# Optimization experiments

Hardware: AMD Instinct MI355X
Metric: run time of the kernel (lower is better)

## Reference

```python
import jax, jax.numpy as jnp
import numpy as np

N_NODES = 1024  # must equal 2*out_channels due to readout(x.T)
N_EDGES = 524288
IN_C, HID_C, OUT_C = 64, 128, 512
MLP_H = 64  # hidden width of EdgeConv MLP


def _linear_init(key, fan_in, fan_out):
    # xavier-normal-like init
    std = (2.0 / (fan_in + fan_out)) ** 0.5
    return jax.random.normal(key, (fan_in, fan_out), dtype=jnp.float32) * std


def setup_inputs() -> dict:
    key = jax.random.key(0)
    ks = jax.random.split(key, 8)
    x = jax.random.normal(ks[0], (N_NODES, IN_C), dtype=jnp.float32)
    edge_index = jax.random.randint(ks[1], (2, N_EDGES), 0, N_NODES, dtype=jnp.int64)
    # conv1 MLP: Linear(2*IN_C, 64) -> ReLU -> Linear(64, HID_C)
    W1 = _linear_init(ks[2], 2 * IN_C, MLP_H); b1 = jnp.zeros((MLP_H,), jnp.float32)
    W2 = _linear_init(ks[3], MLP_H, HID_C);    b2 = jnp.zeros((HID_C,), jnp.float32)
    # conv2 MLP: Linear(2*HID_C, 64) -> ReLU -> Linear(64, OUT_C)
    W3 = _linear_init(ks[4], 2 * HID_C, MLP_H); b3 = jnp.zeros((MLP_H,), jnp.float32)
    W4 = _linear_init(ks[5], MLP_H, OUT_C);     b4 = jnp.zeros((OUT_C,), jnp.float32)
    # readout: Linear(2*OUT_C, OUT_C) applied to x.T (requires N_NODES == 2*OUT_C)
    Wr = _linear_init(ks[6], 2 * OUT_C, OUT_C); br = jnp.zeros((OUT_C,), jnp.float32)
    return {"x": x, "edge_index": edge_index,
            "W1": W1, "b1": b1, "W2": W2, "b2": b2,
            "W3": W3, "b3": b3, "W4": W4, "b4": b4,
            "Wr": Wr, "br": br}


def _edge_conv(x, src, dst, Wa, ba, Wb, bb):
    # message: mlp(cat[x_i, x_j])  with i=target (dst), j=source (src)
    e = jnp.concatenate([x[dst], x[src]], axis=-1)          # [E, 2C]
    m = jnp.maximum(e @ Wa + ba, 0.0) @ Wb + bb             # [E, C_out]
    agg = jax.ops.segment_max(m, dst, num_segments=N_NODES)  # max-aggregate per target node
    # nodes with no incoming edges -> 0 (PyG fill behavior)
    return jnp.where(jnp.isneginf(agg), 0.0, agg)


def reference(x, edge_index, W1, b1, W2, b2, W3, b3, W4, b4, Wr, br):
    src = edge_index[0]
    dst = edge_index[1]
    h = _edge_conv(x, src, dst, W1, b1, W2, b2)   # [N, HID_C]
    h = _edge_conv(h, src, dst, W3, b3, W4, b4)   # [N, OUT_C]
    # readout on h.T: [OUT_C, N] @ [N(=2*OUT_C), OUT_C] -> [OUT_C, OUT_C]
    return h.T @ Wr + br
```

## Files before the change

### kernel.cpp

```cpp
#include <hip/hip_runtime.h>
#include <hip/hip_bf16.h>
#include <float.h>
#include <math.h>

#define N_NODES 1024
#define N_EDGES 524288
#define IN_C    64
#define HID_C   128
#define OUT_C   512
#define MLP_H   64
#define ADJ_WORDS 32
#define KSPLIT  4
#define KCHUNK  (N_NODES / KSPLIT)

typedef __attribute__((ext_vector_type(8))) short short8;
typedef __attribute__((ext_vector_type(4))) float f32x4;

static __device__ __forceinline__ unsigned short f2bf(float f) {
    __hip_bfloat16 h = __float2bfloat16(f);
    return __builtin_bit_cast(unsigned short, h);
}

__global__ void k_zero_adj(unsigned int* __restrict__ adj) {
    int i = blockIdx.x * blockDim.x + threadIdx.x;
    if (i < N_NODES * ADJ_WORDS) adj[i] = 0u;
}

__global__ void k_build_adj(const int* __restrict__ ei, unsigned int* __restrict__ adj) {
    int e = blockIdx.x * blockDim.x + threadIdx.x;
    if (e >= N_EDGES) return;
    int src = ei[e];
    int dst = ei[N_EDGES + e];
    atomicOr(&adj[dst * ADJ_WORDS + (src >> 5)], 1u << (src & 31));
}

__global__ void k_pack_w(const float* __restrict__ W, unsigned short* __restrict__ Wpk, int C) {
    int idx = blockIdx.x * blockDim.x + threadIdx.x;
    int total = (C / 16) * 2 * 64;
    if (idx >= total) return;
    int lane = idx & 63;
    int kf = (idx >> 6) & 1;
    int nt = idx >> 7;
    int kbase = kf * 32 + (lane >> 4) * 8;
    int c = nt * 16 + (lane & 15);
#pragma unroll
    for (int e = 0; e < 8; ++e)
        Wpk[idx * 8 + e] = f2bf(W[(kbase + e) * C + c]);
}

__global__ void k_xform1(const float* __restrict__ x, const float* __restrict__ W1,
                         const float* __restrict__ b1,
                         float* __restrict__ A1, float* __restrict__ B1) {
    int n = blockIdx.x, t = threadIdx.x;
    __shared__ float xs[IN_C];
    xs[t] = x[n * IN_C + t];
    __syncthreads();
    float a = b1[t], b = 0.f;
#pragma unroll
    for (int k = 0; k < IN_C; ++k) {
        float xv = xs[k];
        a = fmaf(xv, W1[k * MLP_H + t], a);
        b = fmaf(xv, W1[(IN_C + k) * MLP_H + t], b);
    }
    A1[n * MLP_H + t] = a;
    B1[n * MLP_H + t] = b;
}

__global__ void k_xform2(const float* __restrict__ h1, const float* __restrict__ W3,
                         const float* __restrict__ b3,
                         float* __restrict__ A2, float* __restrict__ B2) {
    int n = blockIdx.x, t = threadIdx.x;
    __shared__ float hs[HID_C];
    hs[t] = h1[n * HID_C + t];
    hs[t + 64] = h1[n * HID_C + t + 64];
    __syncthreads();
    float a = b3[t], b = 0.f;
#pragma unroll
    for (int k = 0; k < HID_C; ++k) {
        float hv = hs[k];
        a = fmaf(hv, W3[k * MLP_H + t], a);
        b = fmaf(hv, W3[(HID_C + k) * MLP_H + t], b);
    }
    A2[n * MLP_H + t] = a;
    B2[n * MLP_H + t] = b;
}

template <int NTILES, int C_TOTAL>
__global__ __launch_bounds__(256, (NTILES == 2 ? 5 : 4)) void k_conv_mfma(
        const unsigned int* __restrict__ adj,
        const float* __restrict__ Anode, const float* __restrict__ Bnode,
        const unsigned short* __restrict__ Wpk, const float* __restrict__ bias_g,
        float* __restrict__ out) {
    constexpr int BATCH = 4;
    __shared__ unsigned short list[N_NODES + 16];
    __shared__ short8 zbuf[2][BATCH][2][64];
    __shared__ int cnt;
    const int i = blockIdx.x;
    const int tid = threadIdx.x;
    const int lane = tid & 63;
    const int wave = tid >> 6;
    const int g = lane >> 4;
    const int r = lane & 15;

    if (wave == 0) {
        unsigned int bits = (lane < ADJ_WORDS) ? adj[i * ADJ_WORDS + lane] : 0u;
        int c = __popc(bits);
        int pre = c;
#pragma unroll
        for (int d = 1; d < 64; d <<= 1) {
            int t = __shfl_up(pre, d);
            if (lane >= d) pre += t;
        }
        int total = __shfl(pre, 63);
        int pos = pre - c + lane * 0;
        while (bits) {
            int b = __ffs(bits) - 1;
            bits &= bits - 1;
            list[pos++] = (unsigned short)(lane * 32 + b);
        }
        if (lane == 0) cnt = total;
    }
    __syncthreads();
    const int deg = cnt;

    if (deg == 0) {
        if (lane < 16) {
#pragma unroll
            for (int n = 0; n < NTILES; ++n)
                out[i * C_TOTAL + (wave * NTILES + n) * 16 + lane] = 0.f;
        }
        return;
    }

    const int padded = (deg + 15) & ~15;
    for (int p = deg + tid; p < padded; p += 256) list[p] = list[0];

    short8 wfr[NTILES][2];
#pragma unroll
    for (int n = 0; n < NTILES; ++n) {
        int nt = wave * NTILES + n;
#pragma unroll
        for (int kf = 0; kf < 2; ++kf)
            wfr[n][kf] = ((const short8*)Wpk)[(nt * 2 + kf) * 64 + lane];
    }

    const f32x4* Ap = (const f32x4*)(Anode + i * MLP_H);
    f32x4 a0 = Ap[g * 2], a1 = Ap[g * 2 + 1], a2 = Ap[8 + g * 2], a3 = Ap[9 + g * 2];

    float mx[NTILES];
#pragma unroll
    for (int n = 0; n < NTILES; ++n) mx[n] = -INFINITY;

    auto build = [&](int buf, int base_tile, int ntl) {
        if (wave < ntl) {
            int j = list[(base_tile + wave) * 16 + r];
            const f32x4* Bp = (const f32x4*)(Bnode + (size_t)j * MLP_H);
            f32x4 b0 = Bp[g * 2], b1 = Bp[g * 2 + 1], b2 = Bp[8 + g * 2], b3 = Bp[9 + g * 2];
            f32x4 s0 = a0 + b0, s1 = a1 + b1, s2 = a2 + b2, s3 = a3 + b3;
            short8 z0, z1;
#pragma unroll
            for (int e = 0; e < 4; ++e) {
                z0[e]     = (short)f2bf(fmaxf(s0[e], 0.f));
                z0[e + 4] = (short)f2bf(fmaxf(s1[e], 0.f));
                z1[e]     = (short)f2bf(fmaxf(s2[e], 0.f));
                z1[e + 4] = (short)f2bf(fmaxf(s3[e], 0.f));
            }
            zbuf[buf][wave][0][lane] = z0;
            zbuf[buf][wave][1][lane] = z1;
        }
    };

    const int ntiles_e = padded >> 4;
    const f32x4 zero = {0.f, 0.f, 0.f, 0.f};

    __syncthreads();
    build(0, 0, min(BATCH, ntiles_e));
    __syncthreads();

    int cur = 0;
    for (int b0 = 0; b0 < ntiles_e; b0 += BATCH) {
        int nb = min(BATCH, ntiles_e - b0);
        int nxt = b0 + BATCH;
        if (nxt < ntiles_e) build(cur ^ 1, nxt, min(BATCH, ntiles_e - nxt));
        for (int tt = 0; tt < nb; ++tt) {
            short8 z0 = zbuf[cur][tt][0][lane];
            short8 z1 = zbuf[cur][tt][1][lane];
#pragma unroll
            for (int n = 0; n < NTILES; ++n) {
                f32x4 acc = __builtin_amdgcn_mfma_f32_16x16x32_bf16(z0, wfr[n][0], zero, 0, 0, 0);
                acc = __builtin_amdgcn_mfma_f32_16x16x32_bf16(z1, wfr[n][1], acc, 0, 0, 0);
                mx[n] = fmaxf(mx[n], fmaxf(fmaxf(acc[0], acc[1]), fmaxf(acc[2], acc[3])));
            }
        }
        __syncthreads();
        cur ^= 1;
    }

#pragma unroll
    for (int n = 0; n < NTILES; ++n) {
        mx[n] = fmaxf(mx[n], __shfl_xor(mx[n], 16));
        mx[n] = fmaxf(mx[n], __shfl_xor(mx[n], 32));
    }
    if (lane < 16) {
#pragma unroll
        for (int n = 0; n < NTILES; ++n) {
            int c = (wave * NTILES + n) * 16 + lane;
            out[i * C_TOTAL + c] = mx[n] + bias_g[c];
        }
    }
}

__global__ __launch_bounds__(256) void k_readout_part(
        const float* __restrict__ h2, const float* __restrict__ Wr,
        float* __restrict__ partial) {
    __shared__ float As[64][64];
    __shared__ float Bs[64][64];
    const int bid = blockIdx.x;
    const int kc = bid >> 6;
    const int c0 = ((bid >> 3) & 7) * 64;
    const int o0 = (bid & 7) * 64;
    const int k0 = kc * KCHUNK;
    const int tid = threadIdx.x;
    const int tx = tid & 15, ty = tid >> 4;
    float acc[4][4] = {};
    for (int ks = 0; ks < KCHUNK; ks += 64) {
        for (int s = tid; s < 1024; s += 256) {
            int rr = s >> 4;
            int cq = (s & 15) * 4;
            *(float4*)&As[rr][cq] = *(const float4*)&h2[(k0 + ks + rr) * OUT_C + c0 + cq];
            *(float4*)&Bs[rr][cq] = *(const float4*)&Wr[(k0 + ks + rr) * OUT_C + o0 + cq];
        }
        __syncthreads();
#pragma unroll 16
        for (int kk = 0; kk < 64; ++kk) {
            float4 a = *(float4*)&As[kk][ty * 4];
            float4 b = *(float4*)&Bs[kk][tx * 4];
            acc[0][0] = fmaf(a.x, b.x, acc[0][0]); acc[0][1] = fmaf(a.x, b.y, acc[0][1]);
            acc[0][2] = fmaf(a.x, b.z, acc[0][2]); acc[0][3] = fmaf(a.x, b.w, acc[0][3]);
            acc[1][0] = fmaf(a.y, b.x, acc[1][0]); acc[1][1] = fmaf(a.y, b.y, acc[1][1]);
            acc[1][2] = fmaf(a.y, b.z, acc[1][2]); acc[1][3] = fmaf(a.y, b.w, acc[1][3]);
            acc[2][0] = fmaf(a.z, b.x, acc[2][0]); acc[2][1] = fmaf(a.z, b.y, acc[2][1]);
            acc[2][2] = fmaf(a.z, b.z, acc[2][2]); acc[2][3] = fmaf(a.z, b.w, acc[2][3]);
            acc[3][0] = fmaf(a.w, b.x, acc[3][0]); acc[3][1] = fmaf(a.w, b.y, acc[3][1]);
            acc[3][2] = fmaf(a.w, b.z, acc[3][2]); acc[3][3] = fmaf(a.w, b.w, acc[3][3]);
        }
        __syncthreads();
    }
    float* pb = partial + kc * (OUT_C * OUT_C);
#pragma unroll
    for (int u = 0; u < 4; ++u) {
        float4 v = {acc[u][0], acc[u][1], acc[u][2], acc[u][3]};
        *(float4*)&pb[(c0 + ty * 4 + u) * OUT_C + o0 + tx * 4] = v;
    }
}

__global__ __launch_bounds__(256) void k_readout_reduce(
        const float* __restrict__ partial, const float* __restrict__ br,
        float* __restrict__ out) {
    int i = blockIdx.x * 256 + threadIdx.x;
    const float4* p4 = (const float4*)partial;
    float4 s = p4[i];
    float4 t1 = p4[i + 65536];
    float4 t2 = p4[i + 131072];
    float4 t3 = p4[i + 196608];
    s.x += t1.x + t2.x + t3.x;
    s.y += t1.y + t2.y + t3.y;
    s.z += t1.z + t2.z + t3.z;
    s.w += t1.w + t2.w + t3.w;
    float4 b = ((const float4*)br)[i & 127];
    s.x += b.x; s.y += b.y; s.z += b.z; s.w += b.w;
    ((float4*)out)[i] = s;
}

extern "C" void kernel_launch(void* const* d_in, const int* in_sizes, int n_in,
                              void* d_out, int out_size, void* d_ws, size_t ws_size,
                              hipStream_t stream) {
    const float* x  = (const float*)d_in[0];
    const int*   ei = (const int*)d_in[1];
    const float* W1 = (const float*)d_in[2];
    const float* b1 = (const float*)d_in[3];
    const float* W2 = (const float*)d_in[4];
    const float* b2 = (const float*)d_in[5];
    const float* W3 = (const float*)d_in[6];
    const float* b3 = (const float*)d_in[7];
    const float* W4 = (const float*)d_in[8];
    const float* b4 = (const float*)d_in[9];
    const float* Wr = (const float*)d_in[10];
    const float* br = (const float*)d_in[11];
    float* out = (float*)d_out;

    char* ws = (char*)d_ws;
    unsigned int* adj = (unsigned int*)ws;
    float* A1 = (float*)(ws + 131072);
    float* B1 = (float*)(ws + 393216);
    float* h1 = (float*)(ws + 655360);
    float* A2 = (float*)(ws + 1179648);
    float* B2 = (float*)(ws + 1441792);
    float* h2 = (float*)(ws + 1703936);
    unsigned short* Wpk1 = (unsigned short*)(ws + 3801088);
    unsigned short* Wpk2 = (unsigned short*)(ws + 3817472);
    float* partial = (float*)(ws + 3883008);

    k_zero_adj<<<dim3((N_NODES * ADJ_WORDS + 255) / 256), dim3(256), 0, stream>>>(adj);
    k_build_adj<<<dim3(N_EDGES / 256), dim3(256), 0, stream>>>(ei, adj);
    k_pack_w<<<dim3(4), dim3(256), 0, stream>>>(W2, Wpk1, HID_C);
    k_pack_w<<<dim3(16), dim3(256), 0, stream>>>(W4, Wpk2, OUT_C);
    k_xform1<<<dim3(N_NODES), dim3(64), 0, stream>>>(x, W1, b1, A1, B1);
    k_conv_mfma<2, HID_C><<<dim3(N_NODES), dim3(256), 0, stream>>>(adj, A1, B1, Wpk1, b2, h1);
    k_xform2<<<dim3(N_NODES), dim3(64), 0, stream>>>(h1, W3, b3, A2, B2);
    k_conv_mfma<8, OUT_C><<<dim3(N_NODES), dim3(256), 0, stream>>>(adj, A2, B2, Wpk2, b4, h2);
    k_readout_part<<<dim3(64 * KSPLIT), dim3(256), 0, stream>>>(h2, Wr, partial);
    k_readout_reduce<<<dim3(256), dim3(256), 0, stream>>>(partial, br, out);
}
```

Measured before the change: 185.1 us.

## Merge setup kernels, fuse xform2 into conv1, atomic readout reduction

Combines adjacency zeroing, weight packing, the first node transform and bias initialization of the output into one k_init launch. It also fuses the second node transform into the first conv kernel's epilogue so h1 never reaches global memory. The readout's split-K partials are now accumulated with atomicAdd straight into the bias-initialized output, which removes the reduce kernel. The second conv's batch size goes from 4 to 8. Together these cut launch count and intermediate traffic, at the cost of many float atomics and a nondeterministic summation order.

```diff
diff --git a/kernel.cpp b/kernel.cpp
--- a/kernel.cpp
+++ b/kernel.cpp
@@ -21,9 +21,52 @@
     return __builtin_bit_cast(unsigned short, h);
 }
 
-__global__ void k_zero_adj(unsigned int* __restrict__ adj) {
-    int i = blockIdx.x * blockDim.x + threadIdx.x;
-    if (i < N_NODES * ADJ_WORDS) adj[i] = 0u;
+static __device__ __forceinline__ void pack_w_one(
+        const float* __restrict__ W, unsigned short* __restrict__ Wpk, int C, int idx) {
+    int lane = idx & 63;
+    int kf = (idx >> 6) & 1;
+    int nt = idx >> 7;
+    int kbase = kf * 32 + (lane >> 4) * 8;
+    int c = nt * 16 + (lane & 15);
+#pragma unroll
+    for (int e = 0; e < 8; ++e)
+        Wpk[idx * 8 + e] = f2bf(W[(kbase + e) * C + c]);
+}
+
+__global__ __launch_bounds__(256) void k_init(
+        unsigned int* __restrict__ adj,
+        const float* __restrict__ W2, unsigned short* __restrict__ Wpk1,
+        const float* __restrict__ W4, unsigned short* __restrict__ Wpk2,
+        const float* __restrict__ x, const float* __restrict__ W1,
+        const float* __restrict__ b1,
+        float* __restrict__ A1, float* __restrict__ B1,
+        const float* __restrict__ br, float* __restrict__ out) {
+    __shared__ float xs[4][IN_C];
+    const int b = blockIdx.x, tid = threadIdx.x;
+    if (b < 128) {
+        adj[b * 256 + tid] = 0u;
+        return;
+    }
+    if (b < 132) { pack_w_one(W2, Wpk1, HID_C, (b - 128) * 256 + tid); return; }
+    if (b < 148) { pack_w_one(W4, Wpk2, OUT_C, (b - 132) * 256 + tid); return; }
+    if (b < 404) {
+        const int sub = tid >> 6, t = tid & 63;
+        const int n = (b - 148) * 4 + sub;
+        xs[sub][t] = x[n * IN_C + t];
+        __syncthreads();
+        float a = b1[t], bb = 0.f;
+#pragma unroll
+        for (int k = 0; k < IN_C; ++k) {
+            float xv = xs[sub][k];
+            a = fmaf(xv, W1[k * MLP_H + t], a);
+            bb = fmaf(xv, W1[(IN_C + k) * MLP_H + t], bb);
+        }
+        A1[n * MLP_H + t] = a;
+        B1[n * MLP_H + t] = bb;
+        return;
+    }
+    int i4 = (b - 404) * 256 + tid;
+    ((float4*)out)[i4] = ((const float4*)br)[i4 & 127];
 }
 
 __global__ void k_build_adj(const int* __restrict__ ei, unsigned int* __restrict__ adj) {
@@ -34,66 +77,18 @@
     atomicOr(&adj[dst * ADJ_WORDS + (src >> 5)], 1u << (src & 31));
 }
 
-__global__ void k_pack_w(const float* __restrict__ W, unsigned short* __restrict__ Wpk, int C) {
-    int idx = blockIdx.x * blockDim.x + threadIdx.x;
-    int total = (C / 16) * 2 * 64;
-    if (idx >= total) return;
-    int lane = idx & 63;
-    int kf = (idx >> 6) & 1;
-    int nt = idx >> 7;
-    int kbase = kf * 32 + (lane >> 4) * 8;
-    int c = nt * 16 + (lane & 15);
-#pragma unroll
-    for (int e = 0; e < 8; ++e)
-        Wpk[idx * 8 + e] = f2bf(W[(kbase + e) * C + c]);
-}
-
-__global__ void k_xform1(const float* __restrict__ x, const float* __restrict__ W1,
-                         const float* __restrict__ b1,
-                         float* __restrict__ A1, float* __restrict__ B1) {
-    int n = blockIdx.x, t = threadIdx.x;
-    __shared__ float xs[IN_C];
-    xs[t] = x[n * IN_C + t];
-    __syncthreads();
-    float a = b1[t], b = 0.f;
-#pragma unroll
-    for (int k = 0; k < IN_C; ++k) {
-        float xv = xs[k];
-        a = fmaf(xv, W1[k * MLP_H + t], a);
-        b = fmaf(xv, W1[(IN_C + k) * MLP_H + t], b);
-    }
-    A1[n * MLP_H + t] = a;
-    B1[n * MLP_H + t] = b;
-}
-
-__global__ void k_xform2(const float* __restrict__ h1, const float* __restrict__ W3,
-                         const float* __restrict__ b3,
-                         float* __restrict__ A2, float* __restrict__ B2) {
-    int n = blockIdx.x, t = threadIdx.x;
-    __shared__ float hs[HID_C];
-    hs[t] = h1[n * HID_C + t];
-    hs[t + 64] = h1[n * HID_C + t + 64];
-    __syncthreads();
-    float a = b3[t], b = 0.f;
-#pragma unroll
-    for (int k = 0; k < HID_C; ++k) {
-        float hv = hs[k];
-        a = fmaf(hv, W3[k * MLP_H + t], a);
-        b = fmaf(hv, W3[(HID_C + k) * MLP_H + t], b);
-    }
-    A2[n * MLP_H + t] = a;
-    B2[n * MLP_H + t] = b;
-}
-
-template <int NTILES, int C_TOTAL>
-__global__ __launch_bounds__(256, (NTILES == 2 ? 5 : 4)) void k_conv_mfma(
+template <int NTILES, int C_TOTAL, int BATCH, int MINW, bool FUSEX>
+__global__ __launch_bounds__(256, MINW) void k_conv_mfma(
         const unsigned int* __restrict__ adj,
         const float* __restrict__ Anode, const float* __restrict__ Bnode,
         const unsigned short* __restrict__ Wpk, const float* __restrict__ bias_g,
-        float* __restrict__ out) {
-    constexpr int BATCH = 4;
+        float* __restrict__ outv,
+        const float* __restrict__ W3, const float* __restrict__ b3,
+        float* __restrict__ A2out, float* __restrict__ B2out) {
     __shared__ unsigned short list[N_NODES + 16];
     __shared__ short8 zbuf[2][BATCH][2][64];
+    __shared__ float hrow[FUSEX ? HID_C : 1];
+    __shared__ float xsum[FUSEX ? HID_C : 1];
     __shared__ int cnt;
     const int i = blockIdx.x;
     const int tid = threadIdx.x;
@@ -112,7 +107,7 @@
             if (lane >= d) pre += t;
         }
         int total = __shfl(pre, 63);
-        int pos = pre - c + lane * 0;
+        int pos = pre - c;
         while (bits) {
             int b = __ffs(bits) - 1;
             bits &= bits - 1;
@@ -122,16 +117,6 @@
     }
     __syncthreads();
     const int deg = cnt;
-
-    if (deg == 0) {
-        if (lane < 16) {
-#pragma unroll
-            for (int n = 0; n < NTILES; ++n)
-                out[i * C_TOTAL + (wave * NTILES + n) * 16 + lane] = 0.f;
-        }
-        return;
-    }
-
     const int padded = (deg + 15) & ~15;
     for (int p = deg + tid; p < padded; p += 256) list[p] = list[0];
 
@@ -152,21 +137,25 @@
     for (int n = 0; n < NTILES; ++n) mx[n] = -INFINITY;
 
     auto build = [&](int buf, int base_tile, int ntl) {
-        if (wave < ntl) {
-            int j = list[(base_tile + wave) * 16 + r];
-            const f32x4* Bp = (const f32x4*)(Bnode + (size_t)j * MLP_H);
-            f32x4 b0 = Bp[g * 2], b1 = Bp[g * 2 + 1], b2 = Bp[8 + g * 2], b3 = Bp[9 + g * 2];
-            f32x4 s0 = a0 + b0, s1 = a1 + b1, s2 = a2 + b2, s3 = a3 + b3;
-            short8 z0, z1;
-#pragma unroll
-            for (int e = 0; e < 4; ++e) {
-                z0[e]     = (short)f2bf(fmaxf(s0[e], 0.f));
-                z0[e + 4] = (short)f2bf(fmaxf(s1[e], 0.f));
-                z1[e]     = (short)f2bf(fmaxf(s2[e], 0.f));
-                z1[e + 4] = (short)f2bf(fmaxf(s3[e], 0.f));
+#pragma unroll
+        for (int u = 0; u < BATCH / 4; ++u) {
+            int tt = u * 4 + wave;
+            if (tt < ntl) {
+                int j = list[(base_tile + tt) * 16 + r];
+                const f32x4* Bp = (const f32x4*)(Bnode + (size_t)j * MLP_H);
+                f32x4 b0 = Bp[g * 2], b1 = Bp[g * 2 + 1], b2 = Bp[8 + g * 2], b3v = Bp[9 + g * 2];
+                f32x4 s0 = a0 + b0, s1 = a1 + b1, s2 = a2 + b2, s3 = a3 + b3v;
+                short8 z0, z1;
+#pragma unroll
+                for (int e = 0; e < 4; ++e) {
+                    z0[e]     = (short)f2bf(fmaxf(s0[e], 0.f));
+                    z0[e + 4] = (short)f2bf(fmaxf(s1[e], 0.f));
+                    z1[e]     = (short)f2bf(fmaxf(s2[e], 0.f));
+                    z1[e + 4] = (short)f2bf(fmaxf(s3[e], 0.f));
+                }
+                zbuf[buf][tt][0][lane] = z0;
+                zbuf[buf][tt][1][lane] = z1;
             }
-            zbuf[buf][wave][0][lane] = z0;
-            zbuf[buf][wave][1][lane] = z1;
         }
     };
 
@@ -205,14 +194,35 @@
 #pragma unroll
         for (int n = 0; n < NTILES; ++n) {
             int c = (wave * NTILES + n) * 16 + lane;
-            out[i * C_TOTAL + c] = mx[n] + bias_g[c];
+            float hv = (deg == 0) ? 0.f : mx[n] + bias_g[c];
+            if constexpr (FUSEX) hrow[c] = hv;
+            else                 outv[i * C_TOTAL + c] = hv;
+        }
+    }
+
+    if constexpr (FUSEX) {
+        __syncthreads();
+        const int c = tid & 63;
+        const int half = (tid >> 6) & 1;
+        const int ksel = tid >> 7;
+        const float* wp = W3 + (half * 128 + ksel * 64) * MLP_H + c;
+        float s = 0.f;
+#pragma unroll
+        for (int k = 0; k < 64; ++k)
+            s = fmaf(hrow[ksel * 64 + k], wp[k * MLP_H], s);
+        if (ksel) xsum[half * 64 + c] = s;
+        __syncthreads();
+        if (!ksel) {
+            s += xsum[half * 64 + c];
+            if (half == 0) A2out[i * MLP_H + c] = s + b3[c];
+            else           B2out[i * MLP_H + c] = s;
         }
     }
 }
 
 __global__ __launch_bounds__(256) void k_readout_part(
         const float* __restrict__ h2, const float* __restrict__ Wr,
-        float* __restrict__ partial) {
+        float* __restrict__ out) {
     __shared__ float As[64][64];
     __shared__ float Bs[64][64];
     const int bid = blockIdx.x;
@@ -246,30 +256,11 @@
         }
         __syncthreads();
     }
-    float* pb = partial + kc * (OUT_C * OUT_C);
-#pragma unroll
-    for (int u = 0; u < 4; ++u) {
-        float4 v = {acc[u][0], acc[u][1], acc[u][2], acc[u][3]};
-        *(float4*)&pb[(c0 + ty * 4 + u) * OUT_C + o0 + tx * 4] = v;
-    }
-}
-
-__global__ __launch_bounds__(256) void k_readout_reduce(
-        const float* __restrict__ partial, const float* __restrict__ br,
-        float* __restrict__ out) {
-    int i = blockIdx.x * 256 + threadIdx.x;
-    const float4* p4 = (const float4*)partial;
-    float4 s = p4[i];
-    float4 t1 = p4[i + 65536];
-    float4 t2 = p4[i + 131072];
-    float4 t3 = p4[i + 196608];
-    s.x += t1.x + t2.x + t3.x;
-    s.y += t1.y + t2.y + t3.y;
-    s.z += t1.z + t2.z + t3.z;
-    s.w += t1.w + t2.w + t3.w;
-    float4 b = ((const float4*)br)[i & 127];
-    s.x += b.x; s.y += b.y; s.z += b.z; s.w += b.w;
-    ((float4*)out)[i] = s;
+#pragma unroll
+    for (int u = 0; u < 4; ++u)
+#pragma unroll
+        for (int v = 0; v < 4; ++v)
+            atomicAdd(&out[(c0 + ty * 4 + u) * OUT_C + o0 + tx * 4 + v], acc[u][v]);
 }
 
 extern "C" void kernel_launch(void* const* d_in, const int* in_sizes, int n_in,
@@ -293,22 +284,18 @@
     unsigned int* adj = (unsigned int*)ws;
     float* A1 = (float*)(ws + 131072);
     float* B1 = (float*)(ws + 393216);
-    float* h1 = (float*)(ws + 655360);
-    float* A2 = (float*)(ws + 1179648);
-    float* B2 = (float*)(ws + 1441792);
-    float* h2 = (float*)(ws + 1703936);
-    unsigned short* Wpk1 = (unsigned short*)(ws + 3801088);
-    unsigned short* Wpk2 = (unsigned short*)(ws + 3817472);
-    float* partial = (float*)(ws + 3883008);
-
-    k_zero_adj<<<dim3((N_NODES * ADJ_WORDS + 255) / 256), dim3(256), 0, stream>>>(adj);
+    float* A2 = (float*)(ws + 655360);
+    float* B2 = (float*)(ws + 917504);
+    float* h2 = (float*)(ws + 1179648);
+    unsigned short* Wpk1 = (unsigned short*)(ws + 3276800);
+    unsigned short* Wpk2 = (unsigned short*)(ws + 3293184);
+
+    k_init<<<dim3(660), dim3(256), 0, stream>>>(adj, W2, Wpk1, W4, Wpk2,
+                                                x, W1, b1, A1, B1, br, out);
     k_build_adj<<<dim3(N_EDGES / 256), dim3(256), 0, stream>>>(ei, adj);
-    k_pack_w<<<dim3(4), dim3(256), 0, stream>>>(W2, Wpk1, HID_C);
-    k_pack_w<<<dim3(16), dim3(256), 0, stream>>>(W4, Wpk2, OUT_C);
-    k_xform1<<<dim3(N_NODES), dim3(64), 0, stream>>>(x, W1, b1, A1, B1);
-    k_conv_mfma<2, HID_C><<<dim3(N_NODES), dim3(256), 0, stream>>>(adj, A1, B1, Wpk1, b2, h1);
-    k_xform2<<<dim3(N_NODES), dim3(64), 0, stream>>>(h1, W3, b3, A2, B2);
-    k_conv_mfma<8, OUT_C><<<dim3(N_NODES), dim3(256), 0, stream>>>(adj, A2, B2, Wpk2, b4, h2);
-    k_readout_part<<<dim3(64 * KSPLIT), dim3(256), 0, stream>>>(h2, Wr, partial);
-    k_readout_reduce<<<dim3(256), dim3(256), 0, stream>>>(partial, br, out);
-}
+    k_conv_mfma<2, HID_C, 4, 5, true><<<dim3(N_NODES), dim3(256), 0, stream>>>(
+        adj, A1, B1, Wpk1, b2, nullptr, W3, b3, A2, B2);
+    k_conv_mfma<8, OUT_C, 8, 4, false><<<dim3(N_NODES), dim3(256), 0, stream>>>(
+        adj, A2, B2, Wpk2, b4, h2, nullptr, nullptr, nullptr, nullptr);
+    k_readout_part<<<dim3(64 * KSPLIT), dim3(256), 0, stream>>>(h2, Wr, out);
+}
```

Result: slower. 195.3 us (+5.5%).
